# Kernel optimization log

Measured on AMD Instinct MI355X. Metric: run time of the kernel, lower is better.

## Reference

```python
import jax, jax.numpy as jnp
import numpy as np

NEG_INF = -1.0e9  # matches torch masked_fill constant in topk_mean_pooling


def setup_inputs() -> dict:
    key = jax.random.key(0)
    k1, k2 = jax.random.split(key)
    h = jax.random.normal(k1, (8, 4096, 512), dtype=jnp.float32)
    patch_ids = jnp.sort(jax.random.randint(k2, (8, 4096), 0, 1024), axis=-1)
    return {"h": h, "patch_ids": patch_ids, "max_num_patches": 1024, "k": 4}


def reference(h, patch_ids, max_num_patches, k):
    """topk_mean_pooling / pooling_downsample('topk:k') from ByteLatentEncoder.

    h:          [bs, seq_len, dim] float
    patch_ids:  [bs, seq_len] int, values in [0, max_num_patches)
    returns:    [bs, max_num_patches, dim]
    """
    bs, seq_len, dim = h.shape
    P = max_num_patches
    b_idx = jnp.arange(bs)[:, None]  # [bs, 1], broadcasts against patch_ids

    # tokens per patch (one_hot.sum(1) in torch)
    counts = jnp.zeros((bs, P), h.dtype).at[b_idx, patch_ids].add(jnp.ones((), h.dtype))

    h_work = h
    collected = []
    for _ in range(k):  # k is a small fixed constant (from 'topk:N')
        # scatter_reduce(amax, include_self=False): untargeted patches stay 0
        cm = jnp.full((bs, P, dim), -jnp.inf, h.dtype).at[b_idx, patch_ids].max(h_work)
        cm = jnp.where(jnp.isinf(cm), jnp.zeros((), h.dtype), cm)
        collected.append(cm)
        # gather current max back to token positions and knock out all ties
        gathered = cm[b_idx, patch_ids]  # [bs, seq_len, dim]
        h_work = jnp.where(h_work == gathered, jnp.asarray(NEG_INF, h.dtype), h_work)

    topk_vals = jnp.stack(collected, axis=2)  # [bs, P, k, dim]
    # only the first count_p iterations are valid for patch p
    valid = (jnp.arange(k)[None, None, :] < counts[:, :, None]).astype(h.dtype)  # [bs, P, k]
    sum_valid = (topk_vals * valid[..., None]).sum(axis=2)  # [bs, P, dim]
    num_valid = jnp.clip(valid.sum(axis=2), 1.0)[..., None]
    return sum_valid / num_valid
```

## Files before the change

kernel.cpp:

```cpp
#include <hip/hip_runtime.h>
#include <math.h>

#define BS   8
#define SEQ  4096
#define DIM  512
#define NP   1024
#define KTOP 4
#define NEGINF_C (-1.0e9f)

typedef float f32x4 __attribute__((ext_vector_type(4)));

__device__ __forceinline__ void ins5(float v, float& m0, float& m1, float& m2,
                                     float& m3, float& m4) {
    float a;
    a = fmaxf(m0, v); v = fminf(m0, v); m0 = a;
    a = fmaxf(m1, v); v = fminf(m1, v); m1 = a;
    a = fmaxf(m2, v); v = fminf(m2, v); m2 = a;
    a = fmaxf(m3, v); v = fminf(m3, v); m3 = a;
    m4 = fmaxf(m4, v);
}

#define INS5V(v)                                   \
    do {                                           \
        ins5((v).x, a0, a1, a2, a3, a4);           \
        ins5((v).y, b0, b1, b2, b3, b4);           \
        ins5((v).z, c0, c1, c2, c3, c4);           \
        ins5((v).w, d0, d1, d2, d3, d4);           \
    } while (0)

__device__ __forceinline__ float dedup_avg(float s0, float s1, float s2, float s3,
                                           float s4, int n, float inv_n) {
    const bool e1 = (s1 == s0) & (s1 != -INFINITY);
    const bool e2 = (s2 == s1) & (s2 != -INFINITY);
    const bool e3 = (s3 == s2) & (s3 != -INFINITY);
    const float o1 = e1 ? s2 : s1;
    const float o2 = (e1 | e2) ? s3 : s2;
    const float o3 = (e1 | e2 | e3) ? s4 : s3;
    float acc = (s0 == -INFINITY) ? NEGINF_C : s0;
    if (n > 1) acc += (o1 == -INFINITY) ? NEGINF_C : o1;
    if (n > 2) acc += (o2 == -INFINITY) ? NEGINF_C : o2;
    if (n > 3) acc += (o3 == -INFINITY) ? NEGINF_C : o3;
    return acc * inv_n;
}

__global__ __launch_bounds__(128) void topk_pool_kernel(const float* __restrict__ h,
                                                        const int* __restrict__ pid,
                                                        float* __restrict__ out) {
    const int bp = blockIdx.x;
    const int b  = bp >> 10;
    const int p  = bp & (NP - 1);
    const int tid = threadIdx.x;

    const int* ids = pid + b * SEQ;
    const int target = p + (tid & 1);
    int lo = 0, hi = SEQ;
    #pragma unroll
    for (int s = 0; s < 13; ++s) {
        const int mid  = (lo + hi) >> 1;
        const int midc = (mid < SEQ) ? mid : (SEQ - 1);
        const bool go  = (ids[midc] < target) & (mid < hi);
        lo = go ? mid + 1 : lo;
        hi = go ? hi : mid;
    }
    const int start = __shfl(lo, 0);
    const int end   = __shfl(lo, 1);
    const int cnt   = end - start;

    f32x4* outv = (f32x4*)(out + ((size_t)b * NP + p) * DIM);

    if (cnt == 0) {
        __builtin_nontemporal_store((f32x4){0.f, 0.f, 0.f, 0.f}, &outv[tid]);
        return;
    }

    const f32x4* hr = (const f32x4*)(h + (size_t)b * SEQ * DIM)
                      + (size_t)start * (DIM / 4) + tid;

    float a0 = -INFINITY, a1 = -INFINITY, a2 = -INFINITY, a3 = -INFINITY, a4 = -INFINITY;
    float b0 = -INFINITY, b1 = -INFINITY, b2 = -INFINITY, b3 = -INFINITY, b4 = -INFINITY;
    float c0 = -INFINITY, c1 = -INFINITY, c2 = -INFINITY, c3 = -INFINITY, c4 = -INFINITY;
    float d0 = -INFINITY, d1 = -INFINITY, d2 = -INFINITY, d3 = -INFINITY, d4 = -INFINITY;

    int rem = cnt;
    int off = 0;
    for (; rem >= 4; rem -= 4, off += 4 * (DIM / 4)) {
        const f32x4 v0 = hr[off];
        const f32x4 v1 = hr[off + 1 * (DIM / 4)];
        const f32x4 v2 = hr[off + 2 * (DIM / 4)];
        const f32x4 v3 = hr[off + 3 * (DIM / 4)];
        INS5V(v0);
        INS5V(v1);
        INS5V(v2);
        INS5V(v3);
    }
    for (; rem > 0; --rem, off += (DIM / 4)) {
        const f32x4 v = hr[off];
        INS5V(v);
    }

    const int n = (cnt < KTOP) ? cnt : KTOP;
    const float inv_n = 1.0f / (float)n;
    f32x4 r;
    r.x = dedup_avg(a0, a1, a2, a3, a4, n, inv_n);
    r.y = dedup_avg(b0, b1, b2, b3, b4, n, inv_n);
    r.z = dedup_avg(c0, c1, c2, c3, c4, n, inv_n);
    r.w = dedup_avg(d0, d1, d2, d3, d4, n, inv_n);
    __builtin_nontemporal_store(r, &outv[tid]);
}

extern "C" void kernel_launch(void* const* d_in, const int* in_sizes, int n_in,
                              void* d_out, int out_size, void* d_ws, size_t ws_size,
                              hipStream_t stream) {
    const float* h   = (const float*)d_in[0];
    const int*   pid = (const int*)d_in[1];
    float*       out = (float*)d_out;
    (void)d_ws; (void)ws_size;

    topk_pool_kernel<<<dim3(BS * NP), dim3(128), 0, stream>>>(h, pid, out);
}
```

Before: 25.17 us.

## Precompute patch boundaries in separate kernel and batch 8 row loads per iteration

Adds a small preliminary kernel that writes each patch's start offset into workspace, so the pooling kernel reads two ints instead of running a 13-step binary search per block. The main loop now issues 8 clamped row loads at once and masks the out-of-range ones to -inf, increasing memory-level parallelism per patch. The trade-offs are an extra kernel launch, a dependency on the workspace buffer, and wasted loads and compares for patches with few tokens.

```diff
diff --git a/kernel.cpp b/kernel.cpp
--- a/kernel.cpp
+++ b/kernel.cpp
@@ -9,6 +9,22 @@
 #define NEGINF_C (-1.0e9f)
 
 typedef float f32x4 __attribute__((ext_vector_type(4)));
+
+__global__ __launch_bounds__(256) void boundaries_kernel(const int* __restrict__ pid,
+                                                         int* __restrict__ starts) {
+    const int gt = blockIdx.x * 256 + threadIdx.x;
+    const int b  = gt / SEQ;
+    const int t  = gt - b * SEQ;
+    const int* ids = pid + b * SEQ;
+    int* st = starts + b * (NP + 1);
+
+    const int cur  = ids[t];
+    const int prev = (t > 0) ? ids[t - 1] : -1;
+    for (int p = prev + 1; p <= cur; ++p) st[p] = t;
+    if (t == SEQ - 1) {
+        for (int p = cur + 1; p <= NP; ++p) st[p] = SEQ;
+    }
+}
 
 __device__ __forceinline__ void ins5(float v, float& m0, float& m1, float& m2,
                                      float& m3, float& m4) {
@@ -44,26 +60,16 @@
 }
 
 __global__ __launch_bounds__(128) void topk_pool_kernel(const float* __restrict__ h,
-                                                        const int* __restrict__ pid,
+                                                        const int* __restrict__ starts,
                                                         float* __restrict__ out) {
     const int bp = blockIdx.x;
     const int b  = bp >> 10;
     const int p  = bp & (NP - 1);
     const int tid = threadIdx.x;
 
-    const int* ids = pid + b * SEQ;
-    const int target = p + (tid & 1);
-    int lo = 0, hi = SEQ;
-    #pragma unroll
-    for (int s = 0; s < 13; ++s) {
-        const int mid  = (lo + hi) >> 1;
-        const int midc = (mid < SEQ) ? mid : (SEQ - 1);
-        const bool go  = (ids[midc] < target) & (mid < hi);
-        lo = go ? mid + 1 : lo;
-        hi = go ? hi : mid;
-    }
-    const int start = __shfl(lo, 0);
-    const int end   = __shfl(lo, 1);
+    const int* st   = starts + b * (NP + 1);
+    const int start = st[p];
+    const int end   = st[p + 1];
     const int cnt   = end - start;
 
     f32x4* outv = (f32x4*)(out + ((size_t)b * NP + p) * DIM);
@@ -81,21 +87,24 @@
     float c0 = -INFINITY, c1 = -INFINITY, c2 = -INFINITY, c3 = -INFINITY, c4 = -INFINITY;
     float d0 = -INFINITY, d1 = -INFINITY, d2 = -INFINITY, d3 = -INFINITY, d4 = -INFINITY;
 
-    int rem = cnt;
-    int off = 0;
-    for (; rem >= 4; rem -= 4, off += 4 * (DIM / 4)) {
-        const f32x4 v0 = hr[off];
-        const f32x4 v1 = hr[off + 1 * (DIM / 4)];
-        const f32x4 v2 = hr[off + 2 * (DIM / 4)];
-        const f32x4 v3 = hr[off + 3 * (DIM / 4)];
-        INS5V(v0);
-        INS5V(v1);
-        INS5V(v2);
-        INS5V(v3);
-    }
-    for (; rem > 0; --rem, off += (DIM / 4)) {
-        const f32x4 v = hr[off];
-        INS5V(v);
+    const int lastoff = (cnt - 1) * (DIM / 4);
+    for (int t = 0; t < cnt; t += 8) {
+        const int base = t * (DIM / 4);
+        f32x4 v[8];
+        #pragma unroll
+        for (int i = 0; i < 8; ++i) {
+            const int o  = base + i * (DIM / 4);
+            const int oc = (o < lastoff) ? o : lastoff;
+            v[i] = hr[oc];
+        }
+        #pragma unroll
+        for (int i = 0; i < 8; ++i) {
+            if (t + i >= cnt) {
+                v[i].x = -INFINITY; v[i].y = -INFINITY;
+                v[i].z = -INFINITY; v[i].w = -INFINITY;
+            }
+            INS5V(v[i]);
+        }
     }
 
     const int n = (cnt < KTOP) ? cnt : KTOP;
@@ -114,7 +123,8 @@
     const float* h   = (const float*)d_in[0];
     const int*   pid = (const int*)d_in[1];
     float*       out = (float*)d_out;
-    (void)d_ws; (void)ws_size;
+    int*         starts = (int*)d_ws;
 
-    topk_pool_kernel<<<dim3(BS * NP), dim3(128), 0, stream>>>(h, pid, out);
+    boundaries_kernel<<<dim3((BS * SEQ) / 256), dim3(256), 0, stream>>>(pid, starts);
+    topk_pool_kernel<<<dim3(BS * NP), dim3(128), 0, stream>>>(h, starts, out);
 }
```

New measurement: 26.87 us. 6.8% more time.

## Process groups of four patches per block with software-pipelined row streaming

Applied to the files above, without the earlier changes.

Each block now handles four consecutive patches and streams their token rows in a single pass, detecting patch boundaries from the ids, flushing the top-k average at each boundary and zero-filling empty patches. Row loads are double-buffered four at a time so the next batch is in flight while the current one is inserted. This cuts the grid to a quarter of its size, shares one binary search across four patches and keeps loads ahead of the arithmetic. In exchange there is less block-level parallelism, a data-dependent branch inside the loop, and redundant clamped loads at the end of the range.

```diff
diff --git a/kernel.cpp b/kernel.cpp
--- a/kernel.cpp
+++ b/kernel.cpp
@@ -6,6 +6,7 @@
 #define DIM  512
 #define NP   1024
 #define KTOP 4
+#define GRP  4
 #define NEGINF_C (-1.0e9f)
 
 typedef float f32x4 __attribute__((ext_vector_type(4)));
@@ -19,14 +20,6 @@
     a = fmaxf(m3, v); v = fminf(m3, v); m3 = a;
     m4 = fmaxf(m4, v);
 }
-
-#define INS5V(v)                                   \
-    do {                                           \
-        ins5((v).x, a0, a1, a2, a3, a4);           \
-        ins5((v).y, b0, b1, b2, b3, b4);           \
-        ins5((v).z, c0, c1, c2, c3, c4);           \
-        ins5((v).w, d0, d1, d2, d3, d4);           \
-    } while (0)
 
 __device__ __forceinline__ float dedup_avg(float s0, float s1, float s2, float s3,
                                            float s4, int n, float inv_n) {
@@ -43,16 +36,16 @@
     return acc * inv_n;
 }
 
-__global__ __launch_bounds__(128) void topk_pool_kernel(const float* __restrict__ h,
-                                                        const int* __restrict__ pid,
-                                                        float* __restrict__ out) {
-    const int bp = blockIdx.x;
-    const int b  = bp >> 10;
-    const int p  = bp & (NP - 1);
+__global__ __launch_bounds__(128) void topk_stream_kernel(const float* __restrict__ h,
+                                                          const int* __restrict__ pid,
+                                                          float* __restrict__ out) {
+    const int g   = blockIdx.x;
+    const int b   = g >> 8;
+    const int p0  = (g & 255) * GRP;
     const int tid = threadIdx.x;
+    const int* ids = pid + b * SEQ;
 
-    const int* ids = pid + b * SEQ;
-    const int target = p + (tid & 1);
+    const int target = p0 + (tid & 1) * GRP;
     int lo = 0, hi = SEQ;
     #pragma unroll
     for (int s = 0; s < 13; ++s) {
@@ -64,48 +57,86 @@
     }
     const int start = __shfl(lo, 0);
     const int end   = __shfl(lo, 1);
-    const int cnt   = end - start;
 
-    f32x4* outv = (f32x4*)(out + ((size_t)b * NP + p) * DIM);
-
-    if (cnt == 0) {
-        __builtin_nontemporal_store((f32x4){0.f, 0.f, 0.f, 0.f}, &outv[tid]);
-        return;
-    }
-
-    const f32x4* hr = (const f32x4*)(h + (size_t)b * SEQ * DIM)
-                      + (size_t)start * (DIM / 4) + tid;
+    f32x4* outb = (f32x4*)(out + ((size_t)b * NP + p0) * DIM);
+    const f32x4 zv = (f32x4){0.f, 0.f, 0.f, 0.f};
 
     float a0 = -INFINITY, a1 = -INFINITY, a2 = -INFINITY, a3 = -INFINITY, a4 = -INFINITY;
     float b0 = -INFINITY, b1 = -INFINITY, b2 = -INFINITY, b3 = -INFINITY, b4 = -INFINITY;
     float c0 = -INFINITY, c1 = -INFINITY, c2 = -INFINITY, c3 = -INFINITY, c4 = -INFINITY;
     float d0 = -INFINITY, d1 = -INFINITY, d2 = -INFINITY, d3 = -INFINITY, d4 = -INFINITY;
+    int cnt = 0;
+    int cur = p0 - 1;
 
-    int rem = cnt;
-    int off = 0;
-    for (; rem >= 4; rem -= 4, off += 4 * (DIM / 4)) {
-        const f32x4 v0 = hr[off];
-        const f32x4 v1 = hr[off + 1 * (DIM / 4)];
-        const f32x4 v2 = hr[off + 2 * (DIM / 4)];
-        const f32x4 v3 = hr[off + 3 * (DIM / 4)];
-        INS5V(v0);
-        INS5V(v1);
-        INS5V(v2);
-        INS5V(v3);
+#define RESET_ACC()                                                          \
+    do {                                                                     \
+        a0 = a1 = a2 = a3 = a4 = -INFINITY;                                  \
+        b0 = b1 = b2 = b3 = b4 = -INFINITY;                                  \
+        c0 = c1 = c2 = c3 = c4 = -INFINITY;                                  \
+        d0 = d1 = d2 = d3 = d4 = -INFINITY;                                  \
+    } while (0)
+
+#define FLUSH(P)                                                             \
+    do {                                                                     \
+        const int   n_    = (cnt < KTOP) ? cnt : KTOP;                       \
+        const float invn_ = 1.0f / (float)n_;                                \
+        f32x4 r_;                                                            \
+        r_.x = dedup_avg(a0, a1, a2, a3, a4, n_, invn_);                     \
+        r_.y = dedup_avg(b0, b1, b2, b3, b4, n_, invn_);                     \
+        r_.z = dedup_avg(c0, c1, c2, c3, c4, n_, invn_);                     \
+        r_.w = dedup_avg(d0, d1, d2, d3, d4, n_, invn_);                     \
+        __builtin_nontemporal_store(r_, &outb[(size_t)((P) - p0) * (DIM / 4) + tid]); \
+    } while (0)
+
+#define ZERO(P) __builtin_nontemporal_store(zv, &outb[(size_t)((P) - p0) * (DIM / 4) + tid])
+
+    if (start < end) {
+        const f32x4* hb  = (const f32x4*)(h + (size_t)b * SEQ * DIM);
+        const int    lastrow = end - 1;
+
+        f32x4 V[4]; int I[4];
+        #pragma unroll
+        for (int i = 0; i < 4; ++i) {
+            const int tc = (start + i < end) ? start + i : lastrow;
+            V[i] = hb[(size_t)tc * (DIM / 4) + tid];
+            I[i] = ids[tc];
+        }
+
+        for (int t = start; t < end; t += 4) {
+            f32x4 Vn[4]; int In[4];
+            #pragma unroll
+            for (int i = 0; i < 4; ++i) {
+                const int tn = (t + 4 + i < end) ? t + 4 + i : lastrow;
+                Vn[i] = hb[(size_t)tn * (DIM / 4) + tid];
+                In[i] = ids[tn];
+            }
+            #pragma unroll
+            for (int i = 0; i < 4; ++i) {
+                if (t + i < end) {
+                    const int id = I[i];
+                    if (id != cur) {
+                        if (cur >= p0) FLUSH(cur);
+                        for (int q = (cur < p0 ? p0 : cur + 1); q < id; ++q) ZERO(q);
+                        cur = id; cnt = 0;
+                        RESET_ACC();
+                    }
+                    ins5(V[i].x, a0, a1, a2, a3, a4);
+                    ins5(V[i].y, b0, b1, b2, b3, b4);
+                    ins5(V[i].z, c0, c1, c2, c3, c4);
+                    ins5(V[i].w, d0, d1, d2, d3, d4);
+                    ++cnt;
+                }
+            }
+            #pragma unroll
+            for (int i = 0; i < 4; ++i) { V[i] = Vn[i]; I[i] = In[i]; }
+        }
+        FLUSH(cur);
     }
-    for (; rem > 0; --rem, off += (DIM / 4)) {
-        const f32x4 v = hr[off];
-        INS5V(v);
-    }
+    for (int q = (cur < p0 ? p0 : cur + 1); q < p0 + GRP; ++q) ZERO(q);
 
-    const int n = (cnt < KTOP) ? cnt : KTOP;
-    const float inv_n = 1.0f / (float)n;
-    f32x4 r;
-    r.x = dedup_avg(a0, a1, a2, a3, a4, n, inv_n);
-    r.y = dedup_avg(b0, b1, b2, b3, b4, n, inv_n);
-    r.z = dedup_avg(c0, c1, c2, c3, c4, n, inv_n);
-    r.w = dedup_avg(d0, d1, d2, d3, d4, n, inv_n);
-    __builtin_nontemporal_store(r, &outv[tid]);
+#undef RESET_ACC
+#undef FLUSH
+#undef ZERO
 }
 
 extern "C" void kernel_launch(void* const* d_in, const int* in_sizes, int n_in,
@@ -116,5 +147,5 @@
     float*       out = (float*)d_out;
     (void)d_ws; (void)ws_size;
 
-    topk_pool_kernel<<<dim3(BS * NP), dim3(128), 0, stream>>>(h, pid, out);
+    topk_stream_kernel<<<dim3(BS * (NP / GRP)), dim3(128), 0, stream>>>(h, pid, out);
 }
```

Result: slower. 26.95 us (+7.1%).

## Replace binary search with wave-ballot search and add small-patch fast path

Applied to the files above, without the earlier changes.

The serial 13-step binary search over patch_ids is replaced with a three-stage wave-wide ballot search: a coarse probe every 64 entries, a fine probe of 64 entries, and a counting ballot that can extend past 64. This removes a chain of dependent global loads. Patches with at most 4 tokens take a new path that loads each row once and computes the top-k mean directly, with explicit tie handling, instead of running the 5-wide insertion network. The cost is more divergent code and a loop for patches longer than 64 tokens.

```diff
diff --git a/kernel.cpp b/kernel.cpp
--- a/kernel.cpp
+++ b/kernel.cpp
@@ -43,28 +43,54 @@
     return acc * inv_n;
 }
 
+__device__ __forceinline__ float small_avg(float v0, float v1, float v2, float v3,
+                                           int cnt, float inv_n) {
+    const float c1 = (v1 == v0) ? NEGINF_C : v1;
+    const float c2 = ((v2 == v0) | (v2 == v1)) ? NEGINF_C : v2;
+    const float c3 = ((v3 == v0) | (v3 == v1) | (v3 == v2)) ? NEGINF_C : v3;
+    float acc = v0;
+    if (cnt > 1) acc += c1;
+    if (cnt > 2) acc += c2;
+    if (cnt > 3) acc += c3;
+    return acc * inv_n;
+}
+
 __global__ __launch_bounds__(128) void topk_pool_kernel(const float* __restrict__ h,
                                                         const int* __restrict__ pid,
                                                         float* __restrict__ out) {
-    const int bp = blockIdx.x;
-    const int b  = bp >> 10;
-    const int p  = bp & (NP - 1);
-    const int tid = threadIdx.x;
+    const int bp   = blockIdx.x;
+    const int b    = bp >> 10;
+    const int p    = bp & (NP - 1);
+    const int tid  = threadIdx.x;
+    const int lane = tid & 63;
+    const int* ids = pid + b * SEQ;
 
-    const int* ids = pid + b * SEQ;
-    const int target = p + (tid & 1);
-    int lo = 0, hi = SEQ;
-    #pragma unroll
-    for (int s = 0; s < 13; ++s) {
-        const int mid  = (lo + hi) >> 1;
-        const int midc = (mid < SEQ) ? mid : (SEQ - 1);
-        const bool go  = (ids[midc] < target) & (mid < hi);
-        lo = go ? mid + 1 : lo;
-        hi = go ? hi : mid;
+    const int probe1 = lane << 6;
+    const unsigned long long m1 = __ballot(ids[probe1] < p);
+    const int c1 = __popcll(m1);
+    const int base = (c1 == 0) ? 0 : ((c1 - 1) << 6) + 1;
+
+    const int idx2  = base + lane;
+    const int idx2c = (idx2 < SEQ) ? idx2 : (SEQ - 1);
+    const bool lt2  = (idx2 < SEQ) && (ids[idx2c] < p);
+    const int start = base + __popcll(__ballot(lt2));
+
+    const int i3  = start + lane;
+    const int i3c = (i3 < SEQ) ? i3 : (SEQ - 1);
+    const bool eq = (i3 < SEQ) && (ids[i3c] == p);
+    int cnt = __popcll(__ballot(eq));
+    if (cnt == 64) {
+        int off64 = 64;
+        while (true) {
+            const int i  = start + off64 + lane;
+            const int ic = (i < SEQ) ? i : (SEQ - 1);
+            const bool e = (i < SEQ) && (ids[ic] == p);
+            const int cc = __popcll(__ballot(e));
+            cnt += cc;
+            if (cc < 64) break;
+            off64 += 64;
+        }
     }
-    const int start = __shfl(lo, 0);
-    const int end   = __shfl(lo, 1);
-    const int cnt   = end - start;
 
     f32x4* outv = (f32x4*)(out + ((size_t)b * NP + p) * DIM);
 
@@ -75,35 +101,57 @@
 
     const f32x4* hr = (const f32x4*)(h + (size_t)b * SEQ * DIM)
                       + (size_t)start * (DIM / 4) + tid;
+    const int n = (cnt < KTOP) ? cnt : KTOP;
+    const float inv_n = 1.0f / (float)n;
+
+    if (cnt <= KTOP) {
+        const int o1 = ((1 < cnt) ? 1 : (cnt - 1)) * (DIM / 4);
+        const int o2 = ((2 < cnt) ? 2 : (cnt - 1)) * (DIM / 4);
+        const int o3 = ((3 < cnt) ? 3 : (cnt - 1)) * (DIM / 4);
+        const f32x4 v0 = hr[0];
+        const f32x4 v1 = hr[o1];
+        const f32x4 v2 = hr[o2];
+        const f32x4 v3 = hr[o3];
+        f32x4 r;
+        r.x = small_avg(v0.x, v1.x, v2.x, v3.x, cnt, inv_n);
+        r.y = small_avg(v0.y, v1.y, v2.y, v3.y, cnt, inv_n);
+        r.z = small_avg(v0.z, v1.z, v2.z, v3.z, cnt, inv_n);
+        r.w = small_avg(v0.w, v1.w, v2.w, v3.w, cnt, inv_n);
+        __builtin_nontemporal_store(r, &outv[tid]);
+        return;
+    }
 
     float a0 = -INFINITY, a1 = -INFINITY, a2 = -INFINITY, a3 = -INFINITY, a4 = -INFINITY;
     float b0 = -INFINITY, b1 = -INFINITY, b2 = -INFINITY, b3 = -INFINITY, b4 = -INFINITY;
-    float c0 = -INFINITY, c1 = -INFINITY, c2 = -INFINITY, c3 = -INFINITY, c4 = -INFINITY;
+    float c0 = -INFINITY, c1f = -INFINITY, c2 = -INFINITY, c3 = -INFINITY, c4 = -INFINITY;
     float d0 = -INFINITY, d1 = -INFINITY, d2 = -INFINITY, d3 = -INFINITY, d4 = -INFINITY;
 
     int rem = cnt;
     int off = 0;
     for (; rem >= 4; rem -= 4, off += 4 * (DIM / 4)) {
-        const f32x4 v0 = hr[off];
-        const f32x4 v1 = hr[off + 1 * (DIM / 4)];
-        const f32x4 v2 = hr[off + 2 * (DIM / 4)];
-        const f32x4 v3 = hr[off + 3 * (DIM / 4)];
-        INS5V(v0);
-        INS5V(v1);
-        INS5V(v2);
-        INS5V(v3);
+        const f32x4 w0 = hr[off];
+        const f32x4 w1 = hr[off + 1 * (DIM / 4)];
+        const f32x4 w2 = hr[off + 2 * (DIM / 4)];
+        const f32x4 w3 = hr[off + 3 * (DIM / 4)];
+        ins5(w0.x, a0, a1, a2, a3, a4); ins5(w0.y, b0, b1, b2, b3, b4);
+        ins5(w0.z, c0, c1f, c2, c3, c4); ins5(w0.w, d0, d1, d2, d3, d4);
+        ins5(w1.x, a0, a1, a2, a3, a4); ins5(w1.y, b0, b1, b2, b3, b4);
+        ins5(w1.z, c0, c1f, c2, c3, c4); ins5(w1.w, d0, d1, d2, d3, d4);
+        ins5(w2.x, a0, a1, a2, a3, a4); ins5(w2.y, b0, b1, b2, b3, b4);
+        ins5(w2.z, c0, c1f, c2, c3, c4); ins5(w2.w, d0, d1, d2, d3, d4);
+        ins5(w3.x, a0, a1, a2, a3, a4); ins5(w3.y, b0, b1, b2, b3, b4);
+        ins5(w3.z, c0, c1f, c2, c3, c4); ins5(w3.w, d0, d1, d2, d3, d4);
     }
     for (; rem > 0; --rem, off += (DIM / 4)) {
-        const f32x4 v = hr[off];
-        INS5V(v);
+        const f32x4 w = hr[off];
+        ins5(w.x, a0, a1, a2, a3, a4); ins5(w.y, b0, b1, b2, b3, b4);
+        ins5(w.z, c0, c1f, c2, c3, c4); ins5(w.w, d0, d1, d2, d3, d4);
     }
 
-    const int n = (cnt < KTOP) ? cnt : KTOP;
-    const float inv_n = 1.0f / (float)n;
     f32x4 r;
     r.x = dedup_avg(a0, a1, a2, a3, a4, n, inv_n);
     r.y = dedup_avg(b0, b1, b2, b3, b4, n, inv_n);
-    r.z = dedup_avg(c0, c1, c2, c3, c4, n, inv_n);
+    r.z = dedup_avg(c0, c1f, c2, c3, c4, n, inv_n);
     r.w = dedup_avg(d0, d1, d2, d3, d4, n, inv_n);
     __builtin_nontemporal_store(r, &outv[tid]);
 }
```

After: 21.14 us. -16.0%, faster.
